# Kernel tuning notes

Hardware: AMD Instinct MI355X
Metric: run time of the kernel (lower is better)

## Reference

```python
import jax, jax.numpy as jnp
import numpy as np

EPS = 1e-5        # BatchNorm eps (torch default)
ALPHA = 0.2       # LeakyReLU negative slope


def _gather_nbrs(x, idx):
    # x: (B,N,C), idx: (B,P,S) -> (B,P,S,C)
    B, P, S = idx.shape
    flat = jnp.take_along_axis(x, idx.reshape(B, P * S, 1), axis=1)
    return flat.reshape(B, P, S, x.shape[-1])


def _mlp_layer(x, w, b, g, bt, m, v):
    # 1x1 Conv2d == channel matmul; BN in eval mode with running stats; ReLU.
    h = x @ w.T + b
    h = (h - m) * jax.lax.rsqrt(v + EPS) * g + bt
    return jax.nn.relu(h)


def setup_inputs() -> dict:
    key = jax.random.key(0)
    ks = jax.random.split(key, 8)
    B, N, P, S, C = 16, 4096, 1024, 32, 64
    inp = {
        "xyz": jax.random.normal(ks[0], (B, 3, N), dtype=jnp.float32),
        "points": jax.random.normal(ks[1], (B, C, N), dtype=jnp.float32),
        "fps_idx": jax.random.randint(ks[2], (B, P), 0, N, dtype=jnp.int32),
        "group_idx": jax.random.randint(ks[3], (B, P, S), 0, N, dtype=jnp.int32),
    }
    chans = [(64, 67), (64, 64), (128, 64)]
    for i, (co, ci) in enumerate(chans, start=1):
        kk = jax.random.fold_in(key, 100 + i)
        inp[f"w{i}"] = jax.random.normal(kk, (co, ci), dtype=jnp.float32) * (1.0 / np.sqrt(ci))
        inp[f"b{i}"] = jnp.zeros((co,), jnp.float32)
        inp[f"g{i}"] = jnp.ones((co,), jnp.float32)
        inp[f"beta{i}"] = jnp.zeros((co,), jnp.float32)
        inp[f"m{i}"] = jnp.zeros((co,), jnp.float32)
        inp[f"v{i}"] = jnp.ones((co,), jnp.float32)
    inp["a"] = jax.random.normal(ks[4], (3 + 128, 128), dtype=jnp.float32) * 0.1
    return inp


def reference(xyz, points, fps_idx, group_idx,
              w1, b1, g1, beta1, m1, v1,
              w2, b2, g2, beta2, m2, v2,
              w3, b3, g3, beta3, m3, v3, a):
    xyz_p = jnp.transpose(xyz, (0, 2, 1))      # (B,N,3)
    pts_p = jnp.transpose(points, (0, 2, 1))   # (B,N,C)

    # sample_and_group with precomputed fps / ball-query indices
    new_xyz = jnp.take_along_axis(xyz_p, fps_idx[:, :, None], axis=1)   # (B,P,3)
    fps_feat = jnp.take_along_axis(pts_p, fps_idx[:, :, None], axis=1)  # (B,P,C)
    grouped_xyz = _gather_nbrs(xyz_p, group_idx) - new_xyz[:, :, None, :]  # relative (B,P,S,3)
    grouped_feat = _gather_nbrs(pts_p, group_idx)                           # (B,P,S,C)

    new_points = jnp.concatenate([grouped_xyz, grouped_feat], axis=-1)  # (B,P,S,3+C)
    fps_points = jnp.concatenate([new_xyz, fps_feat], axis=-1)          # (B,P,3+C)

    layers = [(w1, b1, g1, beta1, m1, v1), (w2, b2, g2, beta2, m2, v2), (w3, b3, g3, beta3, m3, v3)]
    for (w, b, g, bt, m, v) in layers:
        new_points = _mlp_layer(new_points, w, b, g, bt, m, v)
        fps_points = _mlp_layer(fps_points, w, b, g, bt, m, v)

    # GraphAttention: delta features -> leaky-relu scores -> softmax over neighbors -> pool
    delta_p = new_xyz[:, :, None, :] - grouped_xyz        # (B,P,S,3)
    delta_h = fps_points[:, :, None, :] - new_points       # (B,P,S,D)
    e = jnp.concatenate([delta_p, delta_h], axis=-1) @ a   # (B,P,S,D)
    e = jnp.where(e > 0, e, ALPHA * e)
    attn = jax.nn.softmax(e, axis=2)                       # softmax over nsample
    pooled = jnp.sum(attn * new_points, axis=2)            # (B,P,D)

    return jnp.transpose(new_xyz, (0, 2, 1)), jnp.transpose(pooled, (0, 2, 1))
```

## Files before the change

### kernel.cpp

```cpp
#include <hip/hip_runtime.h>
#include <hip/hip_bf16.h>

#define Bn 16
#define Nn 4096
#define Pn 1024
#define Sn 32
#define Cn 64
#define EPSn 1e-5f
#define ALPHAn 0.2f
#define LOG2E 1.44269504088896341f

#define W1O 0
#define W2O 4352
#define W3O 8448
#define AO  16640
#define B1O 33536
#define B2O 33600
#define B3O 33664
#define WSF 33792
__device__ __align__(16) float g_W[WSF];

#define F1F 0
#define F2F 24
#define F3F 40
#define F5F 72
#define NFRAG 152
#define WFU (NFRAG * 512)
__device__ __align__(16) unsigned short g_Wf[WFU];

__device__ __align__(16) float g_pts[Bn * Nn * 68];
__device__ __align__(16) float g_fps[Bn * Pn * 132];
__device__ __align__(16) float g_tmp[Bn * Pn * 128];

typedef __attribute__((ext_vector_type(8))) short short8;
typedef __attribute__((ext_vector_type(4))) float f32x4;

__device__ __forceinline__ void split2(float v, unsigned short& hu, unsigned short& lu) {
  __hip_bfloat16 h = __float2bfloat16(v);
  float hv = __bfloat162float(h);
  __hip_bfloat16 l = __float2bfloat16(v - hv);
  hu = *(unsigned short*)&h;
  lu = *(unsigned short*)&l;
}
__device__ __forceinline__ unsigned short bfh(float v) {
  __hip_bfloat16 h = __float2bfloat16(v);
  return *(unsigned short*)&h;
}
__device__ __forceinline__ float bf2f(unsigned short u) {
  __hip_bfloat16 h = *(__hip_bfloat16*)&u;
  return __bfloat162float(h);
}

#define MFMA_BF16 __builtin_amdgcn_mfma_f32_16x16x32_bf16
#define TERM3(Ci, Ahh, All, Bh, Bl) \
    Ci = MFMA_BF16(Ahh, Bh, Ci, 0, 0, 0); \
    Ci = MFMA_BF16(Ahh, Bl, Ci, 0, 0, 0); \
    Ci = MFMA_BF16(All, Bh, Ci, 0, 0, 0);

__global__ __launch_bounds__(256) void prep_kernel(
    const float* __restrict__ xyz, const float* __restrict__ points,
    const float* __restrict__ w1, const float* __restrict__ b1,
    const float* __restrict__ g1, const float* __restrict__ bt1,
    const float* __restrict__ m1, const float* __restrict__ v1,
    const float* __restrict__ w2, const float* __restrict__ b2,
    const float* __restrict__ g2, const float* __restrict__ bt2,
    const float* __restrict__ m2, const float* __restrict__ v2,
    const float* __restrict__ w3, const float* __restrict__ b3,
    const float* __restrict__ g3, const float* __restrict__ bt3,
    const float* __restrict__ m3, const float* __restrict__ v3,
    const float* __restrict__ a)
{
  if (blockIdx.x < 1024) {
    __shared__ float T[68 * 65];
    const int t = threadIdx.x;
    const int b = blockIdx.x >> 6, n0 = (blockIdx.x & 63) << 6;
    const int nn = t & 63, cgrp = t >> 6;
    #pragma unroll
    for (int k = 0; k < 16; ++k) {
      const int c = cgrp * 16 + k;
      T[c * 65 + nn] = points[(b * Cn + c) * Nn + n0 + nn];
    }
    if (cgrp == 0) {
      #pragma unroll
      for (int d = 0; d < 3; ++d)
        T[(64 + d) * 65 + nn] = xyz[(b * 3 + d) * Nn + n0 + nn];
      T[67 * 65 + nn] = 0.f;
    }
    __syncthreads();
    const int row = t >> 2, part = t & 3;
    float* dst = g_pts + (((long)b << 12) + n0 + row) * 68 + part * 16;
    #pragma unroll
    for (int j = 0; j < 4; ++j) {
      const int o = part * 16 + j * 4;
      float4 v = { T[(o + 0) * 65 + row], T[(o + 1) * 65 + row],
                   T[(o + 2) * 65 + row], T[(o + 3) * 65 + row] };
      *(float4*)(dst + j * 4) = v;
    }
    if (part == 3) {
      float4 v = { T[64 * 65 + row], T[65 * 65 + row],
                   T[66 * 65 + row], T[67 * 65 + row] };
      *(float4*)(dst + 16) = v;
    }
    return;
  }
  const int idx = (blockIdx.x - 1024) * blockDim.x + threadIdx.x;
  if (idx < WSF) {
    float val;
    if (idx < W2O) {
      const int k = idx >> 6, o = idx & 63;
      const float sc = g1[o] * rsqrtf(v1[o] + EPSn);
      val = (k < 64) ? w1[o * 67 + 3 + k] * sc
          : (k < 67) ? w1[o * 67 + (k - 64)] * sc : 0.f;
    } else if (idx < W3O) {
      const int r = idx - W2O, k = r >> 6, o = r & 63;
      val = w2[o * 64 + k] * (g2[o] * rsqrtf(v2[o] + EPSn));
    } else if (idx < AO) {
      const int r = idx - W3O, k = r >> 7, o = r & 127;
      val = w3[o * 64 + k] * (g3[o] * rsqrtf(v3[o] + EPSn));
    } else if (idx < B1O) {
      int r = idx - AO;
      const int half = r / 8448; r -= half * 8448;
      const int k = r >> 6, o = half * 64 + (r & 63);
      val = (k < 128) ? a[(3 + k) * 128 + o]
          : (k < 131) ? a[(k - 128) * 128 + o] : 0.f;
    } else if (idx < B2O) {
      const int o = idx - B1O;
      val = (b1[o] - m1[o]) * (g1[o] * rsqrtf(v1[o] + EPSn)) + bt1[o];
    } else if (idx < B3O) {
      const int o = idx - B2O;
      val = (b2[o] - m2[o]) * (g2[o] * rsqrtf(v2[o] + EPSn)) + bt2[o];
    } else {
      const int o = idx - B3O;
      val = (b3[o] - m3[o]) * (g3[o] * rsqrtf(v3[o] + EPSn)) + bt3[o];
    }
    g_W[idx] = val;
  } else if (idx < WSF + WFU) {
    const int i = idx - WSF;
    const int frag = i >> 9, r = i & 511;
    const int lane = r >> 3, j = r & 7;
    const int quad = lane >> 4, nn = lane & 15;
    int plane, n, k;
    float w;
    if (frag < F2F) {
      const int f = frag;
      plane = f & 1;
      const int c = (f >> 1) & 1, kcch = f >> 2, kc = kcch % 3, ch = kcch / 3;
      n = ch * 32 + c * 16 + nn; k = kc * 32 + quad * 8 + j;
      const float s = g1[n] * rsqrtf(v1[n] + EPSn);
      w = (k < 64) ? w1[n * 67 + 3 + k] * s
        : (k < 67) ? w1[n * 67 + (k - 64)] * s : 0.f;
    } else if (frag < F3F) {
      const int f = frag - F2F;
      plane = f & 1;
      const int c = (f >> 1) & 1, kc = (f >> 2) & 1, ch = f >> 3;
      n = ch * 32 + c * 16 + nn; k = kc * 32 + quad * 8 + j;
      w = w2[n * 64 + k] * (g2[n] * rsqrtf(v2[n] + EPSn));
    } else if (frag < F5F) {
      const int f = frag - F3F;
      plane = f & 1;
      const int c = (f >> 1) & 3, kc = (f >> 3) & 1, ch = f >> 4;
      n = ch * 64 + c * 16 + nn; k = kc * 32 + quad * 8 + j;
      w = w3[n * 64 + k] * (g3[n] * rsqrtf(v3[n] + EPSn));
    } else {
      const int f = frag - F5F;
      plane = f & 1;
      const int c = (f >> 1) & 3, kcch = f >> 3, kc = kcch % 5, ch = kcch / 5;
      n = ch * 64 + c * 16 + nn; k = kc * 32 + quad * 8 + j;
      w = ((k < 128) ? a[(3 + k) * 128 + n]
        : (k < 131) ? a[(k - 128) * 128 + n] : 0.f) * LOG2E;
    }
    unsigned short hu, lu; split2(w, hu, lu);
    g_Wf[i] = plane ? lu : hu;
  }
}

#define XAs 88
#define XHs 152

__global__ __launch_bounds__(256) void fps_kernel(
    const int* __restrict__ fps_idx, float* __restrict__ out)
{
  __shared__ __align__(16) unsigned char LB[15376];
  unsigned short* XAh = (unsigned short*)(LB + 0);
  unsigned short* XAl = (unsigned short*)(LB + 2816);
  unsigned short* XHh = (unsigned short*)(LB + 5632);
  unsigned short* XHl = (unsigned short*)(LB + 10496);
  unsigned short* ZS  = (unsigned short*)(LB + 15360);

  const int t = threadIdx.x, lane = t & 63, w = t >> 6;
  const int quad = lane >> 4, nn = lane & 15;
  const int ch = w >> 1, cl = w & 1;
  const int blk = ((blockIdx.x & 7) << 7) | (blockIdx.x >> 3);
  const int g0 = blk * 16;

  if (t < 4) ((float*)ZS)[t] = 0.f;

  if (t < 128) {
    const int s0 = t >> 3, cg = t & 7;
    const int gp = g0 + s0, b = gp >> 10, p = gp & 1023;
    const int fi = fps_idx[gp];
    const float* frow = g_pts + (((long)b << 12) + fi) * 68;
    const int c0 = cg * 8;
    const float4 va = *(const float4*)(frow + c0);
    const float4 vb = *(const float4*)(frow + c0 + 4);
    short8 hv, lv;
    unsigned short hu, lu;
    split2(va.x, hu, lu); hv[0] = (short)hu; lv[0] = (short)lu;
    split2(va.y, hu, lu); hv[1] = (short)hu; lv[1] = (short)lu;
    split2(va.z, hu, lu); hv[2] = (short)hu; lv[2] = (short)lu;
    split2(va.w, hu, lu); hv[3] = (short)hu; lv[3] = (short)lu;
    split2(vb.x, hu, lu); hv[4] = (short)hu; lv[4] = (short)lu;
    split2(vb.y, hu, lu); hv[5] = (short)hu; lv[5] = (short)lu;
    split2(vb.z, hu, lu); hv[6] = (short)hu; lv[6] = (short)lu;
    split2(vb.w, hu, lu); hv[7] = (short)hu; lv[7] = (short)lu;
    *(short8*)(XAh + s0 * XAs + c0) = hv;
    *(short8*)(XAl + s0 * XAs + c0) = lv;
    if (cg == 0) {
      #pragma unroll
      for (int d = 0; d < 3; ++d) {
        const float v = frow[64 + d];
        unsigned short h2, l2; split2(v, h2, l2);
        XAh[s0 * XAs + 64 + d] = h2; XAl[s0 * XAs + 64 + d] = l2;
        XHh[s0 * XHs + 128 + d] = h2; XHl[s0 * XHs + 128 + d] = l2;
        out[(b * 3 + d) * Pn + p] = v;
        g_fps[(long)gp * 132 + 128 + d] = v;
      }
    } else if (cg == 1) {
      #pragma unroll
      for (int j = 0; j < 13; ++j) { XAh[s0 * XAs + 67 + j] = 0; XAl[s0 * XAs + 67 + j] = 0; }
    } else if (cg == 2) {
      #pragma unroll
      for (int j = 0; j < 13; ++j) { XHh[s0 * XHs + 131 + j] = 0; XHl[s0 * XHs + 131 + j] = 0; }
    }
  }
  __syncthreads();

  f32x4 C[2];
  const int col1 = w * 16 + nn;

  {
    const float bb = g_W[B1O + col1];
    C[0] = (f32x4){bb, bb, bb, bb};
  }
  #pragma unroll
  for (int kc = 0; kc < 3; ++kc) {
    const int ka = kc * 32 + quad * 8;
    const short8 A0h = (ka < 80) ? *(const short8*)(XAh + nn * XAs + ka) : *(const short8*)ZS;
    const short8 A0l = (ka < 80) ? *(const short8*)(XAl + nn * XAs + ka) : *(const short8*)ZS;
    const unsigned short* pf = g_Wf + (((ch * 3 + kc) * 2 + cl) * 2) * 512 + lane * 8;
    const short8 Bh = *(const short8*)pf, Bl = *(const short8*)(pf + 512);
    TERM3(C[0], A0h, A0l, Bh, Bl);
  }
  #pragma unroll
  for (int r = 0; r < 4; ++r) {
    const float v = fmaxf(C[0][r], 0.f);
    unsigned short hu, lu; split2(v, hu, lu);
    XHh[(quad * 4 + r) * XHs + col1] = hu;
    XHl[(quad * 4 + r) * XHs + col1] = lu;
  }
  __syncthreads();

  {
    const float bb = g_W[B2O + col1];
    C[0] = (f32x4){bb, bb, bb, bb};
  }
  #pragma unroll
  for (int kc = 0; kc < 2; ++kc) {
    const int ka = kc * 32 + quad * 8;
    const short8 A0h = *(const short8*)(XHh + nn * XHs + ka);
    const short8 A0l = *(const short8*)(XHl + nn * XHs + ka);
    const unsigned short* pf = g_Wf + (F2F + ((ch * 2 + kc) * 2 + cl) * 2) * 512 + lane * 8;
    const short8 Bh = *(const short8*)pf, Bl = *(const short8*)(pf + 512);
    TERM3(C[0], A0h, A0l, Bh, Bl);
  }
  __syncthreads();
  #pragma unroll
  for (int r = 0; r < 4; ++r) {
    const float v = fmaxf(C[0][r], 0.f);
    unsigned short hu, lu; split2(v, hu, lu);
    XAh[(quad * 4 + r) * XAs + col1] = hu;
    XAl[(quad * 4 + r) * XAs + col1] = lu;
  }
  __syncthreads();

  {
    const float b0 = g_W[B3O + w * 32 + nn];
    const float b1 = g_W[B3O + w * 32 + 16 + nn];
    C[0] = (f32x4){b0, b0, b0, b0};
    C[1] = (f32x4){b1, b1, b1, b1};
  }
  #pragma unroll
  for (int kc = 0; kc < 2; ++kc) {
    const int ka = kc * 32 + quad * 8;
    const short8 A0h = *(const short8*)(XAh + nn * XAs + ka);
    const short8 A0l = *(const short8*)(XAl + nn * XAs + ka);
    #pragma unroll
    for (int c2 = 0; c2 < 2; ++c2) {
      const unsigned short* pf = g_Wf + (F3F + ((ch * 2 + kc) * 4 + cl * 2 + c2) * 2) * 512 + lane * 8;
      const short8 Bh = *(const short8*)pf, Bl = *(const short8*)(pf + 512);
      TERM3(C[c2], A0h, A0l, Bh, Bl);
    }
  }
  __syncthreads();
  #pragma unroll
  for (int c2 = 0; c2 < 2; ++c2) {
    const int col = w * 32 + c2 * 16 + nn;
    #pragma unroll
    for (int r = 0; r < 4; ++r) {
      const float v = fmaxf(C[c2][r], 0.f);
      unsigned short hu, lu; split2(v, hu, lu);
      XHh[(quad * 4 + r) * XHs + col] = hu;
      XHl[(quad * 4 + r) * XHs + col] = lu;
    }
  }
  __syncthreads();

  C[0] = (f32x4){0.f,0.f,0.f,0.f}; C[1] = C[0];
  #pragma unroll
  for (int kc = 0; kc < 5; ++kc) {
    const int ka = kc * 32 + quad * 8;
    const short8 A0h = (ka < 144) ? *(const short8*)(XHh + nn * XHs + ka) : *(const short8*)ZS;
    const short8 A0l = (ka < 144) ? *(const short8*)(XHl + nn * XHs + ka) : *(const short8*)ZS;
    #pragma unroll
    for (int c2 = 0; c2 < 2; ++c2) {
      const unsigned short* pf = g_Wf + (F5F + ((ch * 5 + kc) * 4 + cl * 2 + c2) * 2) * 512 + lane * 8;
      const short8 Bh = *(const short8*)pf, Bl = *(const short8*)(pf + 512);
      TERM3(C[c2], A0h, A0l, Bh, Bl);
    }
  }
  #pragma unroll
  for (int c2 = 0; c2 < 2; ++c2) {
    const int col = w * 32 + c2 * 16 + nn;
    #pragma unroll
    for (int r = 0; r < 4; ++r)
      g_fps[(long)(g0 + quad * 4 + r) * 132 + col] = C[c2][r];
  }
}

__global__ __launch_bounds__(256) void transpose_out(float* __restrict__ out)
{
  __shared__ float T[64 * 129];
  const int t = threadIdx.x;
  const int b = blockIdx.x >> 4, p0 = (blockIdx.x & 15) << 6;
  const int c = t & 127, ph = t >> 7;
  #pragma unroll
  for (int pp = 0; pp < 32; ++pp) {
    const int pi = ph * 32 + pp;
    T[pi * 129 + c] = g_tmp[(((long)b << 10) + p0 + pi) * 128 + c];
  }
  __syncthreads();
  const int pn = t & 63, cg = t >> 6;
  #pragma unroll
  for (int k = 0; k < 32; ++k) {
    const int cc = cg * 32 + k;
    out[Bn * 3 * Pn + ((b << 7) + cc) * Pn + p0 + pn] = T[pn * 129 + cc];
  }
}

#define OXB0 0
#define OXB1 9728
#define OZS  19456
#define LDSB 19472

#define FS_PTR(XBg, cc) ((float*)((XBg) + ((cc) >> 2) * XHs + 144 + ((cc) & 3) * 2))

__global__ __launch_bounds__(256, 6) void fused_kernel(
    const int* __restrict__ group_idx)
{
  __shared__ __align__(16) unsigned char LB[LDSB];
  unsigned short* const XB0 = (unsigned short*)(LB + OXB0);
  unsigned short* const XB1 = (unsigned short*)(LB + OXB1);
  unsigned short* ZS = (unsigned short*)(LB + OZS);

  const int t = threadIdx.x, lane = t & 63, w = t >> 6;
  const int quad = lane >> 4, nn = lane & 15;
  const int ch = w >> 1, cl = w & 1;
  const int blk = ((blockIdx.x & 7) << 10) | (blockIdx.x >> 3);
  const int base = blk * 2;
  const int b = base >> 10;

  {
    const int gi = t >> 7, cc = t & 127;
    unsigned short* XBg = gi ? XB1 : XB0;
    *FS_PTR(XBg, cc) = g_fps[(long)(base + gi) * 132 + cc];
  }
  if (t < 4) ((float*)ZS)[t] = 0.f;

  {
    const int s0 = t >> 3, cg = t & 7;
    const int c0 = cg * 8;
    #pragma unroll
    for (int gi = 0; gi < 2; ++gi) {
      unsigned short* XBg = gi ? XB1 : XB0;
      const int gidx = group_idx[(base + gi) * Sn + s0];
      const float* prow = g_pts + (((long)b << 12) + gidx) * 68;
      const float4 va = *(const float4*)(prow + c0);
      const float4 vb = *(const float4*)(prow + c0 + 4);
      unsigned q0, q1, q2, q3;
      asm("v_cvt_pk_bf16_f32 %0, %1, %2" : "=v"(q0) : "v"(va.x), "v"(va.y));
      asm("v_cvt_pk_bf16_f32 %0, %1, %2" : "=v"(q1) : "v"(va.z), "v"(va.w));
      asm("v_cvt_pk_bf16_f32 %0, %1, %2" : "=v"(q2) : "v"(vb.x), "v"(vb.y));
      asm("v_cvt_pk_bf16_f32 %0, %1, %2" : "=v"(q3) : "v"(vb.z), "v"(vb.w));
      uint4 hv = {q0, q1, q2, q3};
      *(uint4*)(XBg + s0 * XHs + c0) = hv;
      if (cg == 0) {
        #pragma unroll
        for (int d = 0; d < 3; ++d) {
          const float r = prow[64 + d] - g_fps[(long)(base + gi) * 132 + 128 + d];
          const unsigned short hu = bfh(r);
          XBg[s0 * XHs + 64 + d] = hu;
          XBg[s0 * XHs + 128 + d] = hu;
        }
      } else if (cg == 1) {
        #pragma unroll
        for (int j = 0; j < 15; ++j) XBg[s0 * XHs + 67 + j] = 0;
      } else if (cg == 2) {
        #pragma unroll
        for (int j = 0; j < 14; ++j) XBg[s0 * XHs + 82 + j] = 0;
      } else if (cg == 3) {
        #pragma unroll
        for (int j = 0; j < 13; ++j) XBg[s0 * XHs + 131 + j] = 0;
      }
    }
  }
  __syncthreads();

  const int col1 = w * 16 + nn;

  {
    f32x4 C00, C01, C10, C11;
    const float bb = g_W[B1O + col1];
    C00 = (f32x4){bb, bb, bb, bb};
    C01 = C00; C10 = C00; C11 = C00;
    #pragma unroll
    for (int kc = 0; kc < 3; ++kc) {
      const int ka = kc * 32 + quad * 8;
      const unsigned short* pf = g_Wf + (((ch * 3 + kc) * 2 + cl) * 2) * 512 + lane * 8;
      const short8 Bh = *(const short8*)pf, Bl = *(const short8*)(pf + 512);
      const short8 A00 = *(const short8*)(XB0 + nn * XHs + ka);
      const short8 A01 = *(const short8*)(XB0 + (16 + nn) * XHs + ka);
      const short8 A10 = *(const short8*)(XB1 + nn * XHs + ka);
      const short8 A11 = *(const short8*)(XB1 + (16 + nn) * XHs + ka);
      C00 = MFMA_BF16(A00, Bh, C00, 0, 0, 0);
      C00 = MFMA_BF16(A00, Bl, C00, 0, 0, 0);
      C01 = MFMA_BF16(A01, Bh, C01, 0, 0, 0);
      C01 = MFMA_BF16(A01, Bl, C01, 0, 0, 0);
      C10 = MFMA_BF16(A10, Bh, C10, 0, 0, 0);
      C10 = MFMA_BF16(A10, Bl, C10, 0, 0, 0);
      C11 = MFMA_BF16(A11, Bh, C11, 0, 0, 0);
      C11 = MFMA_BF16(A11, Bl, C11, 0, 0, 0);
    }
    __syncthreads();
    #pragma unroll
    for (int r = 0; r < 4; ++r) {
      XB0[(quad * 4 + r) * XHs + col1]      = bfh(fmaxf(C00[r], 0.f));
      XB0[(16 + quad * 4 + r) * XHs + col1] = bfh(fmaxf(C01[r], 0.f));
      XB1[(quad * 4 + r) * XHs + col1]      = bfh(fmaxf(C10[r], 0.f));
      XB1[(16 + quad * 4 + r) * XHs + col1] = bfh(fmaxf(C11[r], 0.f));
    }
  }
  __syncthreads();

  {
    f32x4 C00, C01, C10, C11;
    const float bb = g_W[B2O + col1];
    C00 = (f32x4){bb, bb, bb, bb};
    C01 = C00; C10 = C00; C11 = C00;
    #pragma unroll
    for (int kc = 0; kc < 2; ++kc) {
      const int ka = kc * 32 + quad * 8;
      const unsigned short* pf = g_Wf + (F2F + ((ch * 2 + kc) * 2 + cl) * 2) * 512 + lane * 8;
      const short8 Bh = *(const short8*)pf, Bl = *(const short8*)(pf + 512);
      const short8 A00 = *(const short8*)(XB0 + nn * XHs + ka);
      const short8 A01 = *(const short8*)(XB0 + (16 + nn) * XHs + ka);
      const short8 A10 = *(const short8*)(XB1 + nn * XHs + ka);
      const short8 A11 = *(const short8*)(XB1 + (16 + nn) * XHs + ka);
      C00 = MFMA_BF16(A00, Bh, C00, 0, 0, 0);
      C00 = MFMA_BF16(A00, Bl, C00, 0, 0, 0);
      C01 = MFMA_BF16(A01, Bh, C01, 0, 0, 0);
      C01 = MFMA_BF16(A01, Bl, C01, 0, 0, 0);
      C10 = MFMA_BF16(A10, Bh, C10, 0, 0, 0);
      C10 = MFMA_BF16(A10, Bl, C10, 0, 0, 0);
      C11 = MFMA_BF16(A11, Bh, C11, 0, 0, 0);
      C11 = MFMA_BF16(A11, Bl, C11, 0, 0, 0);
    }
    #pragma unroll
    for (int r = 0; r < 4; ++r) {
      XB0[(quad * 4 + r) * XHs + 64 + col1]      = bfh(fmaxf(C00[r], 0.f));
      XB0[(16 + quad * 4 + r) * XHs + 64 + col1] = bfh(fmaxf(C01[r], 0.f));
      XB1[(quad * 4 + r) * XHs + 64 + col1]      = bfh(fmaxf(C10[r], 0.f));
      XB1[(16 + quad * 4 + r) * XHs + 64 + col1] = bfh(fmaxf(C11[r], 0.f));
    }
  }
  __syncthreads();

  {
    f32x4 C0[4], C1[4];
    const float b0 = g_W[B3O + w * 32 + nn];
    const float b1 = g_W[B3O + w * 32 + 16 + nn];
    C0[0] = (f32x4){b0, b0, b0, b0};
    C0[1] = (f32x4){b1, b1, b1, b1};
    C0[2] = C0[0]; C0[3] = C0[1];
    C1[0] = C0[0]; C1[1] = C0[1]; C1[2] = C0[0]; C1[3] = C0[1];
    #pragma unroll
    for (int kc = 0; kc < 2; ++kc) {
      const int ka = 64 + kc * 32 + quad * 8;
      const short8 A00 = *(const short8*)(XB0 + nn * XHs + ka);
      const short8 A01 = *(const short8*)(XB0 + (16 + nn) * XHs + ka);
      const short8 A10 = *(const short8*)(XB1 + nn * XHs + ka);
      const short8 A11 = *(const short8*)(XB1 + (16 + nn) * XHs + ka);
      #pragma unroll
      for (int c2 = 0; c2 < 2; ++c2) {
        const unsigned short* pf = g_Wf + (F3F + ((ch * 2 + kc) * 4 + cl * 2 + c2) * 2) * 512 + lane * 8;
        const short8 Bh = *(const short8*)pf, Bl = *(const short8*)(pf + 512);
        C0[0 + c2] = MFMA_BF16(A00, Bh, C0[0 + c2], 0, 0, 0);
        C0[0 + c2] = MFMA_BF16(A00, Bl, C0[0 + c2], 0, 0, 0);
        C0[2 + c2] = MFMA_BF16(A01, Bh, C0[2 + c2], 0, 0, 0);
        C0[2 + c2] = MFMA_BF16(A01, Bl, C0[2 + c2], 0, 0, 0);
        C1[0 + c2] = MFMA_BF16(A10, Bh, C1[0 + c2], 0, 0, 0);
        C1[0 + c2] = MFMA_BF16(A10, Bl, C1[0 + c2], 0, 0, 0);
        C1[2 + c2] = MFMA_BF16(A11, Bh, C1[2 + c2], 0, 0, 0);
        C1[2 + c2] = MFMA_BF16(A11, Bl, C1[2 + c2], 0, 0, 0);
      }
    }
    __syncthreads();
    #pragma unroll
    for (int c2 = 0; c2 < 2; ++c2) {
      const int col = w * 32 + c2 * 16 + nn;
      #pragma unroll
      for (int r = 0; r < 4; ++r) {
        XB0[(quad * 4 + r) * XHs + col]      = bfh(fmaxf(C0[0 + c2][r], 0.f));
        XB0[(16 + quad * 4 + r) * XHs + col] = bfh(fmaxf(C0[2 + c2][r], 0.f));
        XB1[(quad * 4 + r) * XHs + col]      = bfh(fmaxf(C1[0 + c2][r], 0.f));
        XB1[(16 + quad * 4 + r) * XHs + col] = bfh(fmaxf(C1[2 + c2][r], 0.f));
      }
    }
  }
  __syncthreads();

  f32x4 C0[4], C1[4];
  {
    const float e00 = *FS_PTR(XB0, w * 32 + nn);
    const float e01 = *FS_PTR(XB0, w * 32 + 16 + nn);
    const float e10 = *FS_PTR(XB1, w * 32 + nn);
    const float e11 = *FS_PTR(XB1, w * 32 + 16 + nn);
    C0[0] = (f32x4){-e00, -e00, -e00, -e00};
    C0[1] = (f32x4){-e01, -e01, -e01, -e01};
    C0[2] = C0[0]; C0[3] = C0[1];
    C1[0] = (f32x4){-e10, -e10, -e10, -e10};
    C1[1] = (f32x4){-e11, -e11, -e11, -e11};
    C1[2] = C1[0]; C1[3] = C1[1];
  }
  #pragma unroll
  for (int kc = 0; kc < 5; ++kc) {
    const int ka = kc * 32 + quad * 8;
    const short8 A00 = (ka < 144) ? *(const short8*)(XB0 + nn * XHs + ka) : *(const short8*)ZS;
    const short8 A01 = (ka < 144) ? *(const short8*)(XB0 + (16 + nn) * XHs + ka) : *(const short8*)ZS;
    const short8 A10 = (ka < 144) ? *(const short8*)(XB1 + nn * XHs + ka) : *(const short8*)ZS;
    const short8 A11 = (ka < 144) ? *(const short8*)(XB1 + (16 + nn) * XHs + ka) : *(const short8*)ZS;
    #pragma unroll
    for (int c2 = 0; c2 < 2; ++c2) {
      const unsigned short* pf = g_Wf + (F5F + ((ch * 5 + kc) * 4 + cl * 2 + c2) * 2) * 512 + lane * 8;
      const short8 Bh = *(const short8*)pf, Bl = *(const short8*)(pf + 512);
      C0[0 + c2] = MFMA_BF16(A00, Bh, C0[0 + c2], 0, 0, 0);
      C0[0 + c2] = MFMA_BF16(A00, Bl, C0[0 + c2], 0, 0, 0);
      C0[2 + c2] = MFMA_BF16(A01, Bh, C0[2 + c2], 0, 0, 0);
      C0[2 + c2] = MFMA_BF16(A01, Bl, C0[2 + c2], 0, 0, 0);
      C1[0 + c2] = MFMA_BF16(A10, Bh, C1[0 + c2], 0, 0, 0);
      C1[0 + c2] = MFMA_BF16(A10, Bl, C1[0 + c2], 0, 0, 0);
      C1[2 + c2] = MFMA_BF16(A11, Bh, C1[2 + c2], 0, 0, 0);
      C1[2 + c2] = MFMA_BF16(A11, Bl, C1[2 + c2], 0, 0, 0);
    }
  }

  #pragma unroll
  for (int gi = 0; gi < 2; ++gi) {
    unsigned short* XBg = gi ? XB1 : XB0;
    #pragma unroll
    for (int c2 = 0; c2 < 2; ++c2) {
      const int col = w * 32 + c2 * 16 + nn;
      f32x4* Cg = gi ? C1 : C0;
      float tmin = 3.4e38f;
      #pragma unroll
      for (int mi = 0; mi < 2; ++mi)
        #pragma unroll
        for (int r = 0; r < 4; ++r) {
          const int idx = mi * 2 + c2;
          const float cv = Cg[idx][r];
          const float tv = fminf(cv, 0.2f * cv);
          Cg[idx][r] = tv;
          tmin = fminf(tmin, tv);
        }
      tmin = fminf(tmin, __shfl_xor(tmin, 16));
      tmin = fminf(tmin, __shfl_xor(tmin, 32));
      float den = 0.f, pool = 0.f;
      #pragma unroll
      for (int mi = 0; mi < 2; ++mi)
        #pragma unroll
        for (int r = 0; r < 4; ++r) {
          const int idx = mi * 2 + c2;
          const float wgt = __builtin_amdgcn_exp2f(tmin - Cg[idx][r]);
          den += wgt;
          pool = fmaf(wgt, bf2f(XBg[(mi * 16 + quad * 4 + r) * XHs + col]), pool);
        }
      den  += __shfl_xor(den, 16);  den  += __shfl_xor(den, 32);
      pool += __shfl_xor(pool, 16); pool += __shfl_xor(pool, 32);
      if (quad == 0)
        g_tmp[(long)(base + gi) * 128 + col] =
            pool * __builtin_amdgcn_rcpf(den);
    }
  }
}

extern "C" void kernel_launch(void* const* d_in, const int* in_sizes, int n_in,
                              void* d_out, int out_size, void* d_ws, size_t ws_size,
                              hipStream_t stream) {
  const float* xyz       = (const float*)d_in[0];
  const float* points    = (const float*)d_in[1];
  const int*   fps_idx   = (const int*)d_in[2];
  const int*   group_idx = (const int*)d_in[3];

  const int prep_blocks = 1024 + (WSF + WFU + 255) / 256;
  prep_kernel<<<prep_blocks, 256, 0, stream>>>(
      xyz, points,
      (const float*)d_in[4],  (const float*)d_in[5],
      (const float*)d_in[6],  (const float*)d_in[7],
      (const float*)d_in[8],  (const float*)d_in[9],
      (const float*)d_in[10], (const float*)d_in[11],
      (const float*)d_in[12], (const float*)d_in[13],
      (const float*)d_in[14], (const float*)d_in[15],
      (const float*)d_in[16], (const float*)d_in[17],
      (const float*)d_in[18], (const float*)d_in[19],
      (const float*)d_in[20], (const float*)d_in[21],
      (const float*)d_in[22]);

  fps_kernel<<<1024, 256, 0, stream>>>(fps_idx, (float*)d_out);

  fused_kernel<<<Bn * Pn / 2, 256, 0, stream>>>(group_idx);

  transpose_out<<<Bn * 16, 256, 0, stream>>>((float*)d_out);
}
```

Baseline: 221.2 us.

## XOR-swizzle fused kernel LDS tiles and halve fps_kernel rows per block

Applies an XOR swizzle on columns within the bf16 activation tiles in the fused kernel. Rows 8-15 of each 16-row group get their columns flipped by 16, which is meant to cut LDS bank conflicts on MFMA operand reads and result writes. Separately, fps_kernel now handles 8 points per block instead of 16 and launches twice as many blocks, so half the MFMA rows are padding. This adds parallelism for the small fps stage at the cost of wasted compute.

```diff
diff --git a/kernel.cpp b/kernel.cpp
--- a/kernel.cpp
+++ b/kernel.cpp
@@ -190,12 +190,12 @@
   const int t = threadIdx.x, lane = t & 63, w = t >> 6;
   const int quad = lane >> 4, nn = lane & 15;
   const int ch = w >> 1, cl = w & 1;
-  const int blk = ((blockIdx.x & 7) << 7) | (blockIdx.x >> 3);
-  const int g0 = blk * 16;
+  const int blk = ((blockIdx.x & 7) << 8) | (blockIdx.x >> 3);
+  const int g0 = blk * 8;
 
   if (t < 4) ((float*)ZS)[t] = 0.f;
 
-  if (t < 128) {
+  if (t < 64) {
     const int s0 = t >> 3, cg = t & 7;
     const int gp = g0 + s0, b = gp >> 10, p = gp & 1023;
     const int fi = fps_idx[gp];
@@ -328,12 +328,14 @@
       TERM3(C[c2], A0h, A0l, Bh, Bl);
     }
   }
-  #pragma unroll
-  for (int c2 = 0; c2 < 2; ++c2) {
-    const int col = w * 32 + c2 * 16 + nn;
-    #pragma unroll
-    for (int r = 0; r < 4; ++r)
-      g_fps[(long)(g0 + quad * 4 + r) * 132 + col] = C[c2][r];
+  if (quad < 2) {
+    #pragma unroll
+    for (int c2 = 0; c2 < 2; ++c2) {
+      const int col = w * 32 + c2 * 16 + nn;
+      #pragma unroll
+      for (int r = 0; r < 4; ++r)
+        g_fps[(long)(g0 + quad * 4 + r) * 132 + col] = C[c2][r];
+    }
   }
 }
 
@@ -379,6 +381,9 @@
   const int base = blk * 2;
   const int b = base >> 10;
 
+  const int rswA = (nn & 8) << 1;
+  const int rswC = (quad & 2) << 3;
+
   {
     const int gi = t >> 7, cc = t & 127;
     unsigned short* XBg = gi ? XB1 : XB0;
@@ -388,6 +393,7 @@
 
   {
     const int s0 = t >> 3, cg = t & 7;
+    const int rswS = (s0 & 8) << 1;
     const int c0 = cg * 8;
     #pragma unroll
     for (int gi = 0; gi < 2; ++gi) {
@@ -402,21 +408,21 @@
       asm("v_cvt_pk_bf16_f32 %0, %1, %2" : "=v"(q2) : "v"(vb.x), "v"(vb.y));
       asm("v_cvt_pk_bf16_f32 %0, %1, %2" : "=v"(q3) : "v"(vb.z), "v"(vb.w));
       uint4 hv = {q0, q1, q2, q3};
-      *(uint4*)(XBg + s0 * XHs + c0) = hv;
+      *(uint4*)(XBg + s0 * XHs + (c0 ^ rswS)) = hv;
       if (cg == 0) {
         #pragma unroll
         for (int d = 0; d < 3; ++d) {
           const float r = prow[64 + d] - g_fps[(long)(base + gi) * 132 + 128 + d];
           const unsigned short hu = bfh(r);
-          XBg[s0 * XHs + 64 + d] = hu;
+          XBg[s0 * XHs + ((64 + d) ^ rswS)] = hu;
           XBg[s0 * XHs + 128 + d] = hu;
         }
       } else if (cg == 1) {
         #pragma unroll
-        for (int j = 0; j < 15; ++j) XBg[s0 * XHs + 67 + j] = 0;
+        for (int j = 0; j < 15; ++j) XBg[s0 * XHs + ((67 + j) ^ rswS)] = 0;
       } else if (cg == 2) {
         #pragma unroll
-        for (int j = 0; j < 14; ++j) XBg[s0 * XHs + 82 + j] = 0;
+        for (int j = 0; j < 14; ++j) XBg[s0 * XHs + ((82 + j) ^ rswS)] = 0;
       } else if (cg == 3) {
         #pragma unroll
         for (int j = 0; j < 13; ++j) XBg[s0 * XHs + 131 + j] = 0;
@@ -426,6 +432,7 @@
   __syncthreads();
 
   const int col1 = w * 16 + nn;
+  const int col1C = col1 ^ rswC;
 
   {
     f32x4 C00, C01, C10, C11;
@@ -434,7 +441,7 @@
     C01 = C00; C10 = C00; C11 = C00;
     #pragma unroll
     for (int kc = 0; kc < 3; ++kc) {
-      const int ka = kc * 32 + quad * 8;
+      const int ka = (kc * 32 + quad * 8) ^ rswA;
       const unsigned short* pf = g_Wf + (((ch * 3 + kc) * 2 + cl) * 2) * 512 + lane * 8;
       const short8 Bh = *(const short8*)pf, Bl = *(const short8*)(pf + 512);
       const short8 A00 = *(const short8*)(XB0 + nn * XHs + ka);
@@ -453,10 +460,10 @@
     __syncthreads();
     #pragma unroll
     for (int r = 0; r < 4; ++r) {
-      XB0[(quad * 4 + r) * XHs + col1]      = bfh(fmaxf(C00[r], 0.f));
-      XB0[(16 + quad * 4 + r) * XHs + col1] = bfh(fmaxf(C01[r], 0.f));
-      XB1[(quad * 4 + r) * XHs + col1]      = bfh(fmaxf(C10[r], 0.f));
-      XB1[(16 + quad * 4 + r) * XHs + col1] = bfh(fmaxf(C11[r], 0.f));
+      XB0[(quad * 4 + r) * XHs + col1C]      = bfh(fmaxf(C00[r], 0.f));
+      XB0[(16 + quad * 4 + r) * XHs + col1C] = bfh(fmaxf(C01[r], 0.f));
+      XB1[(quad * 4 + r) * XHs + col1C]      = bfh(fmaxf(C10[r], 0.f));
+      XB1[(16 + quad * 4 + r) * XHs + col1C] = bfh(fmaxf(C11[r], 0.f));
     }
   }
   __syncthreads();
@@ -468,7 +475,7 @@
     C01 = C00; C10 = C00; C11 = C00;
     #pragma unroll
     for (int kc = 0; kc < 2; ++kc) {
-      const int ka = kc * 32 + quad * 8;
+      const int ka = (kc * 32 + quad * 8) ^ rswA;
       const unsigned short* pf = g_Wf + (F2F + ((ch * 2 + kc) * 2 + cl) * 2) * 512 + lane * 8;
       const short8 Bh = *(const short8*)pf, Bl = *(const short8*)(pf + 512);
       const short8 A00 = *(const short8*)(XB0 + nn * XHs + ka);
@@ -486,10 +493,10 @@
     }
     #pragma unroll
     for (int r = 0; r < 4; ++r) {
-      XB0[(quad * 4 + r) * XHs + 64 + col1]      = bfh(fmaxf(C00[r], 0.f));
-      XB0[(16 + quad * 4 + r) * XHs + 64 + col1] = bfh(fmaxf(C01[r], 0.f));
-      XB1[(quad * 4 + r) * XHs + 64 + col1]      = bfh(fmaxf(C10[r], 0.f));
-      XB1[(16 + quad * 4 + r) * XHs + 64 + col1] = bfh(fmaxf(C11[r], 0.f));
+      XB0[(quad * 4 + r) * XHs + 64 + col1C]      = bfh(fmaxf(C00[r], 0.f));
+      XB0[(16 + quad * 4 + r) * XHs + 64 + col1C] = bfh(fmaxf(C01[r], 0.f));
+      XB1[(quad * 4 + r) * XHs + 64 + col1C]      = bfh(fmaxf(C10[r], 0.f));
+      XB1[(16 + quad * 4 + r) * XHs + 64 + col1C] = bfh(fmaxf(C11[r], 0.f));
     }
   }
   __syncthreads();
@@ -504,7 +511,7 @@
     C1[0] = C0[0]; C1[1] = C0[1]; C1[2] = C0[0]; C1[3] = C0[1];
     #pragma unroll
     for (int kc = 0; kc < 2; ++kc) {
-      const int ka = 64 + kc * 32 + quad * 8;
+      const int ka = (64 + kc * 32 + quad * 8) ^ rswA;
       const short8 A00 = *(const short8*)(XB0 + nn * XHs + ka);
       const short8 A01 = *(const short8*)(XB0 + (16 + nn) * XHs + ka);
       const short8 A10 = *(const short8*)(XB1 + nn * XHs + ka);
@@ -526,13 +533,13 @@
     __syncthreads();
     #pragma unroll
     for (int c2 = 0; c2 < 2; ++c2) {
-      const int col = w * 32 + c2 * 16 + nn;
+      const int colC = (w * 32 + c2 * 16 + nn) ^ rswC;
       #pragma unroll
       for (int r = 0; r < 4; ++r) {
-        XB0[(quad * 4 + r) * XHs + col]      = bfh(fmaxf(C0[0 + c2][r], 0.f));
-        XB0[(16 + quad * 4 + r) * XHs + col] = bfh(fmaxf(C0[2 + c2][r], 0.f));
-        XB1[(quad * 4 + r) * XHs + col]      = bfh(fmaxf(C1[0 + c2][r], 0.f));
-        XB1[(16 + quad * 4 + r) * XHs + col] = bfh(fmaxf(C1[2 + c2][r], 0.f));
+        XB0[(quad * 4 + r) * XHs + colC]      = bfh(fmaxf(C0[0 + c2][r], 0.f));
+        XB0[(16 + quad * 4 + r) * XHs + colC] = bfh(fmaxf(C0[2 + c2][r], 0.f));
+        XB1[(quad * 4 + r) * XHs + colC]      = bfh(fmaxf(C1[0 + c2][r], 0.f));
+        XB1[(16 + quad * 4 + r) * XHs + colC] = bfh(fmaxf(C1[2 + c2][r], 0.f));
       }
     }
   }
@@ -553,11 +560,12 @@
   }
   #pragma unroll
   for (int kc = 0; kc < 5; ++kc) {
-    const int ka = kc * 32 + quad * 8;
-    const short8 A00 = (ka < 144) ? *(const short8*)(XB0 + nn * XHs + ka) : *(const short8*)ZS;
-    const short8 A01 = (ka < 144) ? *(const short8*)(XB0 + (16 + nn) * XHs + ka) : *(const short8*)ZS;
-    const short8 A10 = (ka < 144) ? *(const short8*)(XB1 + nn * XHs + ka) : *(const short8*)ZS;
-    const short8 A11 = (ka < 144) ? *(const short8*)(XB1 + (16 + nn) * XHs + ka) : *(const short8*)ZS;
+    const int kaL = kc * 32 + quad * 8;
+    const int ka = (kaL < 128) ? (kaL ^ rswA) : kaL;
+    const short8 A00 = (kaL < 144) ? *(const short8*)(XB0 + nn * XHs + ka) : *(const short8*)ZS;
+    const short8 A01 = (kaL < 144) ? *(const short8*)(XB0 + (16 + nn) * XHs + ka) : *(const short8*)ZS;
+    const short8 A10 = (kaL < 144) ? *(const short8*)(XB1 + nn * XHs + ka) : *(const short8*)ZS;
+    const short8 A11 = (kaL < 144) ? *(const short8*)(XB1 + (16 + nn) * XHs + ka) : *(const short8*)ZS;
     #pragma unroll
     for (int c2 = 0; c2 < 2; ++c2) {
       const unsigned short* pf = g_Wf + (F5F + ((ch * 5 + kc) * 4 + cl * 2 + c2) * 2) * 512 + lane * 8;
@@ -579,6 +587,7 @@
     #pragma unroll
     for (int c2 = 0; c2 < 2; ++c2) {
       const int col = w * 32 + c2 * 16 + nn;
+      const int colC = col ^ rswC;
       f32x4* Cg = gi ? C1 : C0;
       float tmin = 3.4e38f;
       #pragma unroll
@@ -601,7 +610,7 @@
           const int idx = mi * 2 + c2;
           const float wgt = __builtin_amdgcn_exp2f(tmin - Cg[idx][r]);
           den += wgt;
-          pool = fmaf(wgt, bf2f(XBg[(mi * 16 + quad * 4 + r) * XHs + col]), pool);
+          pool = fmaf(wgt, bf2f(XBg[(mi * 16 + quad * 4 + r) * XHs + colC]), pool);
         }
       den  += __shfl_xor(den, 16);  den  += __shfl_xor(den, 32);
       pool += __shfl_xor(pool, 16); pool += __shfl_xor(pool, 32);
@@ -634,7 +643,7 @@
       (const float*)d_in[20], (const float*)d_in[21],
       (const float*)d_in[22]);
 
-  fps_kernel<<<1024, 256, 0, stream>>>(fps_idx, (float*)d_out);
+  fps_kernel<<<2048, 256, 0, stream>>>(fps_idx, (float*)d_out);
 
   fused_kernel<<<Bn * Pn / 2, 256, 0, stream>>>(group_idx);
 
```

After: 229.8 us. 1.04x slower.
